# Optimization experiments

Measured on AMD Instinct MI355X. Metric: run time of the kernel, lower is better.

Reference implementation:

```python
import jax, jax.numpy as jnp
import numpy as np

B, T, C = 2, 2048, 1024
H, HS = 16, 64          # num_heads, head_size; H*HS == C
FF = 4 * C
EPS = 1e-5


def setup_inputs() -> dict:
    key = jax.random.key(0)
    ks = jax.random.split(key, 10)
    s = 0.02
    return {
        "x": jax.random.normal(ks[0], (B, T, C), dtype=jnp.float32),
        "Wq": jax.random.normal(ks[1], (H, C, HS), dtype=jnp.float32) * s,
        "Wk": jax.random.normal(ks[2], (H, C, HS), dtype=jnp.float32) * s,
        "Wv": jax.random.normal(ks[3], (H, C, HS), dtype=jnp.float32) * s,
        "p": jnp.ones((H,), dtype=jnp.float32),  # per-head learnable scale, init 1
        "Wproj": jax.random.normal(ks[4], (C, C), dtype=jnp.float32) * s,
        "W1": jax.random.normal(ks[5], (C, FF), dtype=jnp.float32) * s,
        "W2": jax.random.normal(ks[6], (FF, C), dtype=jnp.float32) * s,
        "ln1_w": jnp.ones((C,), dtype=jnp.float32),
        "ln1_b": jnp.zeros((C,), dtype=jnp.float32),
        "ln2_w": jnp.ones((C,), dtype=jnp.float32),
        "ln2_b": jnp.zeros((C,), dtype=jnp.float32),
    }


def _layernorm(x, w, b):
    mu = jnp.mean(x, axis=-1, keepdims=True)
    var = jnp.mean(jnp.square(x - mu), axis=-1, keepdims=True)
    return (x - mu) * jax.lax.rsqrt(var + EPS) * w + b


def reference(x, Wq, Wk, Wv, p, Wproj, W1, W2, ln1_w, ln1_b, ln2_w, ln2_b):
    # --- multi-head causal self-attention (dropout p=0 -> identity) ---
    h = _layernorm(x, ln1_w, ln1_b)
    q = jnp.einsum("btc,hcs->bhts", h, Wq)  # [B,H,T,HS]
    k = jnp.einsum("btc,hcs->bhts", h, Wk)
    v = jnp.einsum("btc,hcs->bhts", h, Wv)
    scale = p ** (-0.5)  # per-head scale, p init to 1
    wei = jnp.einsum("bhts,bhks->bhtk", q, k) * scale[None, :, None, None]
    causal = jnp.tril(jnp.ones((T, T), dtype=bool))
    wei = jnp.where(causal[None, None], wei, -jnp.inf)
    wei = jax.nn.softmax(wei, axis=-1)
    att = jnp.einsum("bhtk,bhks->bhts", wei, v)          # [B,H,T,HS]
    att = att.transpose(0, 2, 1, 3).reshape(B, T, C)     # concat heads
    sa = att @ Wproj
    x = x + sa
    # --- feed-forward (activation_id=0 -> ReLU) ---
    h2 = _layernorm(x, ln2_w, ln2_b)
    ff = jax.nn.relu(h2 @ W1) @ W2
    return x + ff
```

## Files before the change

kernel.cpp:

```cpp
#include <hip/hip_runtime.h>


typedef _Float16 f16;
typedef _Float16 f16x8 __attribute__((ext_vector_type(8)));
typedef _Float16 f16x4v __attribute__((ext_vector_type(4)));
typedef float f32x4 __attribute__((ext_vector_type(4)));

static constexpr int Tn = 2048;
static constexpr int Cn = 1024;
static constexpr int HSn = 64;

__device__ __forceinline__ void glds16(const f16* g, f16* l) {
    __builtin_amdgcn_global_load_lds((const __attribute__((address_space(1))) void*)g,
                                     (__attribute__((address_space(3))) void*)l,
                                     16, 0, 0);
}

__device__ __forceinline__ int xcd_swz(int wg, int nwg) {
    int cpx = nwg >> 3;
    return (wg & 7) * cpx + (wg >> 3);
}

__global__ __launch_bounds__(256) void ln_kernel(const float* __restrict__ x,
                                                 const float* __restrict__ w,
                                                 const float* __restrict__ b,
                                                 f16* __restrict__ out) {
    int row = blockIdx.x;
    const float* xr = x + (size_t)row * Cn;
    int tid = threadIdx.x, l = tid & 63, wv = tid >> 6;
    float4 v = *(const float4*)(xr + tid * 4);
    float s = v.x + v.y + v.z + v.w;
    float sq = v.x * v.x + v.y * v.y + v.z * v.z + v.w * v.w;
#pragma unroll
    for (int off = 32; off > 0; off >>= 1) {
        s += __shfl_down(s, off);
        sq += __shfl_down(sq, off);
    }
    __shared__ float red[8];
    if (l == 0) { red[wv] = s; red[wv + 4] = sq; }
    __syncthreads();
    float ts = red[0] + red[1] + red[2] + red[3];
    float tq = red[4] + red[5] + red[6] + red[7];
    float mean = ts * (1.0f / Cn);
    float var = tq * (1.0f / Cn) - mean * mean;
    float rstd = rsqrtf(var + 1e-5f);
    float4 wv4 = *(const float4*)(w + tid * 4);
    float4 bv4 = *(const float4*)(b + tid * 4);
    f16x4v o;
    o[0] = (f16)((v.x - mean) * rstd * wv4.x + bv4.x);
    o[1] = (f16)((v.y - mean) * rstd * wv4.y + bv4.y);
    o[2] = (f16)((v.z - mean) * rstd * wv4.z + bv4.z);
    o[3] = (f16)((v.w - mean) * rstd * wv4.w + bv4.w);
    *(f16x4v*)(out + (size_t)row * Cn + tid * 4) = o;
}

__global__ __launch_bounds__(256) void tr_cast_f32(const float* __restrict__ in, int irs,
                                                   f16* __restrict__ out, int ors) {
    __shared__ float tile[32][33];
    int r0 = blockIdx.x * 32, c0 = blockIdx.y * 32;
    int t = threadIdx.x;
    int rr = t >> 3, c4 = (t & 7) * 4;
    float4 v = *(const float4*)(in + (size_t)(r0 + rr) * irs + c0 + c4);
    tile[rr][c4] = v.x; tile[rr][c4 + 1] = v.y; tile[rr][c4 + 2] = v.z; tile[rr][c4 + 3] = v.w;
    __syncthreads();
    int cc = t >> 3, r4 = (t & 7) * 4;
    f16x4v o;
    o[0] = (f16)tile[r4][cc];
    o[1] = (f16)tile[r4 + 1][cc];
    o[2] = (f16)tile[r4 + 2][cc];
    o[3] = (f16)tile[r4 + 3][cc];
    *(f16x4v*)(out + (size_t)(c0 + cc) * ors + r0 + r4) = o;
}

__global__ __launch_bounds__(256) void tr_cast_qkv(const float* __restrict__ Wq,
                                                   const float* __restrict__ Wk,
                                                   const float* __restrict__ Wv,
                                                   f16* __restrict__ out) {
    int z = blockIdx.z;
    int qkv = z >> 4, h = z & 15;
    const float* in = (qkv == 0 ? Wq : qkv == 1 ? Wk : Wv) + (size_t)h * Cn * HSn;
    f16* o = out + (size_t)(qkv * Cn + h * HSn) * Cn;
    __shared__ float tile[32][33];
    int r0 = blockIdx.x * 32, c0 = blockIdx.y * 32;
    int t = threadIdx.x;
    int rr = t >> 3, c4 = (t & 7) * 4;
    float4 v = *(const float4*)(in + (size_t)(r0 + rr) * HSn + c0 + c4);
    tile[rr][c4] = v.x; tile[rr][c4 + 1] = v.y; tile[rr][c4 + 2] = v.z; tile[rr][c4 + 3] = v.w;
    __syncthreads();
    int cc = t >> 3, r4 = (t & 7) * 4;
    f16x4v ov;
    ov[0] = (f16)tile[r4][cc];
    ov[1] = (f16)tile[r4 + 1][cc];
    ov[2] = (f16)tile[r4 + 2][cc];
    ov[3] = (f16)tile[r4 + 3][cc];
    *(f16x4v*)(o + (size_t)(c0 + cc) * Cn + r0 + r4) = ov;
}

__global__ __launch_bounds__(256) void tr_vT(const f16* __restrict__ QKV, f16* __restrict__ vT) {
    int bh = blockIdx.z;
    int b = bh >> 4, h = bh & 15;
    const f16* in = QKV + (size_t)b * Tn * 3072 + 2048 + h * HSn;
    f16* out = vT + (size_t)bh * HSn * Tn;
    int r0 = blockIdx.x * 64;
    __shared__ __align__(16) f16 tile[64][72];
    int t = threadIdx.x;
#pragma unroll
    for (int i = 0; i < 2; i++) {
        int f = i * 256 + t;
        int rr = f >> 3, c8 = (f & 7) * 8;
        *(uint4*)(&tile[rr][c8]) = *(const uint4*)(in + (size_t)(r0 + rr) * 3072 + c8);
    }
    __syncthreads();
#pragma unroll
    for (int i = 0; i < 2; i++) {
        int f = i * 256 + t;
        int cc = f >> 3, r8 = (f & 7) * 8;
        union { f16 h[8]; uint4 v; } u;
#pragma unroll
        for (int j = 0; j < 8; j++) u.h[j] = tile[r8 + j][cc];
        *(uint4*)(out + (size_t)cc * Tn + r0 + r8) = u.v;
    }
}

template <int EPI>
__global__ __launch_bounds__(256) void gemm_bt(const f16* __restrict__ A, const f16* __restrict__ Bt,
                                               void* __restrict__ Cout, const float* __restrict__ resid,
                                               int M, int N, int K) {
    __shared__ __align__(16) f16 As[2][4096];
    __shared__ __align__(16) f16 Bs[2][4096];
    int nwgx = gridDim.x;
    int sw = xcd_swz(blockIdx.y * nwgx + blockIdx.x, nwgx * gridDim.y);
    int bm = sw % nwgx, bn = sw / nwgx;
    int tid = threadIdx.x, l = tid & 63, w = tid >> 6;
    int wr = w >> 1, wc = w & 1;
    f32x4 acc[4][4];
#pragma unroll
    for (int m = 0; m < 4; m++)
#pragma unroll
        for (int n = 0; n < 4; n++) acc[m][n] = f32x4{0.f, 0.f, 0.f, 0.f};

    const f16* ag = A + (size_t)(bm * 128 + (tid >> 2)) * K + (tid & 3) * 8;
    const f16* bg = Bt + (size_t)(bn * 128 + (tid >> 2)) * K + (tid & 3) * 8;
    const size_t half = (size_t)64 * K;
    int KT = K >> 5;
    int rbase = (wr * 64 + (l & 15)) * 32 + (l >> 4) * 8;
    int cbase = (wc * 64 + (l & 15)) * 32 + (l >> 4) * 8;

    auto stage = [&](int kt, int bf) {
        int k0 = kt * 32;
        glds16(ag + k0, &As[bf][w * 512]);
        glds16(ag + half + k0, &As[bf][2048 + w * 512]);
        glds16(bg + k0, &Bs[bf][w * 512]);
        glds16(bg + half + k0, &Bs[bf][2048 + w * 512]);
    };

    stage(0, 0);
    __syncthreads();
    for (int kt = 0; kt < KT; ++kt) {
        int cb = kt & 1;
        if (kt + 1 < KT) stage(kt + 1, cb ^ 1);
        f16x8 af[4], bfr[4];
#pragma unroll
        for (int m = 0; m < 4; m++) af[m] = *(const f16x8*)(&As[cb][rbase + m * 512]);
#pragma unroll
        for (int n = 0; n < 4; n++) bfr[n] = *(const f16x8*)(&Bs[cb][cbase + n * 512]);
#pragma unroll
        for (int m = 0; m < 4; m++)
#pragma unroll
            for (int n = 0; n < 4; n++)
                acc[m][n] = __builtin_amdgcn_mfma_f32_16x16x32_f16(af[m], bfr[n], acc[m][n], 0, 0, 0);
        __syncthreads();
    }

    int row0 = bm * 128 + wr * 64 + (l >> 4) * 4;
    int col0 = bn * 128 + wc * 64 + (l & 15);
#pragma unroll
    for (int m = 0; m < 4; m++) {
#pragma unroll
        for (int n = 0; n < 4; n++) {
#pragma unroll
            for (int r = 0; r < 4; r++) {
                size_t idx = (size_t)(row0 + m * 16 + r) * N + (col0 + n * 16);
                float v = acc[m][n][r];
                if constexpr (EPI == 0) ((f16*)Cout)[idx] = (f16)v;
                else if constexpr (EPI == 1) ((f16*)Cout)[idx] = (f16)fmaxf(v, 0.f);
                else ((float*)Cout)[idx] = v + resid[idx];
            }
        }
    }
}

template <int EPI>
__global__ __launch_bounds__(512) void gemm_ks(const f16* __restrict__ A, const f16* __restrict__ Bt,
                                               void* __restrict__ Cout, const float* __restrict__ resid,
                                               int M, int N, int K) {
    __shared__ __align__(16) char smem[65536];
    f16* As = (f16*)smem;
    f16* Bs = (f16*)(smem + 32768);
    int nwgx = gridDim.x;
    int sw = xcd_swz(blockIdx.y * nwgx + blockIdx.x, nwgx * gridDim.y);
    int bm = sw % nwgx, bn = sw / nwgx;
    int tid = threadIdx.x, l = tid & 63, w = tid >> 6;
    int grp = w >> 2, wl = w & 3;
    int wr = wl >> 1, wc = wl & 1;
    int Kh = K >> 1;
    int KT = Kh >> 5;

    f32x4 acc[4][4];
#pragma unroll
    for (int m = 0; m < 4; m++)
#pragma unroll
        for (int n = 0; n < 4; n++) acc[m][n] = f32x4{0.f, 0.f, 0.f, 0.f};

    const f16* agp = A + (size_t)(bm * 128 + wl * 16 + (l >> 2)) * K + grp * Kh + (l & 3) * 8;
    const f16* bgp = Bt + (size_t)(bn * 128 + wl * 16 + (l >> 2)) * K + grp * Kh + (l & 3) * 8;
    const size_t half = (size_t)64 * K;
    f16* Ab = As + grp * 8192;
    f16* Bb = Bs + grp * 8192;

    auto stage = [&](int kt, int bf) {
        size_t k0 = (size_t)kt * 32;
        glds16(agp + k0, Ab + bf * 4096 + wl * 512);
        glds16(agp + half + k0, Ab + bf * 4096 + 2048 + wl * 512);
        glds16(bgp + k0, Bb + bf * 4096 + wl * 512);
        glds16(bgp + half + k0, Bb + bf * 4096 + 2048 + wl * 512);
    };

    int rbase = (wr * 64 + (l & 15)) * 32 + (l >> 4) * 8;
    int cbase = (wc * 64 + (l & 15)) * 32 + (l >> 4) * 8;

    stage(0, 0);
    __syncthreads();
    for (int kt = 0; kt < KT; ++kt) {
        int cb = kt & 1;
        if (kt + 1 < KT) stage(kt + 1, cb ^ 1);
        f16x8 af[4], bfr[4];
#pragma unroll
        for (int m = 0; m < 4; m++) af[m] = *(const f16x8*)(Ab + cb * 4096 + rbase + m * 512);
#pragma unroll
        for (int n = 0; n < 4; n++) bfr[n] = *(const f16x8*)(Bb + cb * 4096 + cbase + n * 512);
#pragma unroll
        for (int m = 0; m < 4; m++)
#pragma unroll
            for (int n = 0; n < 4; n++)
                acc[m][n] = __builtin_amdgcn_mfma_f32_16x16x32_f16(af[m], bfr[n], acc[m][n], 0, 0, 0);
        __syncthreads();
    }

    float* red = (float*)smem;
#pragma unroll
    for (int m = 0; m < 4; m++) {
        if (grp == 1) {
#pragma unroll
            for (int n = 0; n < 4; n++)
                *(f32x4*)(red + wl * 1280 + l * 20 + n * 4) = acc[m][n];
        }
        __syncthreads();
        if (grp == 0) {
#pragma unroll
            for (int n = 0; n < 4; n++)
                acc[m][n] += *(const f32x4*)(red + wl * 1280 + l * 20 + n * 4);
        }
        __syncthreads();
    }

    if (grp == 0) {
        int row0 = bm * 128 + wr * 64 + (l >> 4) * 4;
        int col0 = bn * 128 + wc * 64 + (l & 15);
#pragma unroll
        for (int m = 0; m < 4; m++) {
#pragma unroll
            for (int n = 0; n < 4; n++) {
#pragma unroll
                for (int r = 0; r < 4; r++) {
                    size_t idx = (size_t)(row0 + m * 16 + r) * N + (col0 + n * 16);
                    float v = acc[m][n][r];
                    if constexpr (EPI == 0) ((f16*)Cout)[idx] = (f16)v;
                    else if constexpr (EPI == 1) ((f16*)Cout)[idx] = (f16)fmaxf(v, 0.f);
                    else ((float*)Cout)[idx] = v + resid[idx];
                }
            }
        }
    }
}

__global__ __launch_bounds__(256) void attn_kernel(const f16* __restrict__ QKV,
                                                   const f16* __restrict__ vT,
                                                   const float* __restrict__ p,
                                                   f16* __restrict__ att) {
    int sw = xcd_swz(blockIdx.x, gridDim.x);
    int pq = sw & 15, bh = sw >> 4;
    int b = bh >> 4, h = bh & 15;
    int tid = threadIdx.x, w = tid >> 6, l = tid & 63;
    float scale = rsqrtf(p[h]);

    __shared__ __align__(16) f16 Ks[2][4096];
    __shared__ __align__(16) f16 Vs[2][4096];
    __shared__ __align__(16) f16 Ps[4][16 * 80];
    f16* Pw = &Ps[w][0];

    int srow0 = tid >> 3;
    int c0 = (tid & 7) ^ (srow0 & 7);
    int srow1 = 32 + srow0;
    int c1 = (tid & 7) ^ (srow1 & 7);
    const f16* Kg = QKV + (size_t)b * Tn * 3072 + 1024 + h * HSn;
    const f16* Vg = vT + (size_t)bh * HSn * Tn;

    auto stageKV = [&](int kv0, int bf) {
        glds16(Kg + (size_t)(kv0 + srow0) * 3072 + c0 * 8, &Ks[bf][w * 512]);
        glds16(Kg + (size_t)(kv0 + srow1) * 3072 + c1 * 8, &Ks[bf][2048 + w * 512]);
        glds16(Vg + (size_t)srow0 * Tn + kv0 + c0 * 8, &Vs[bf][w * 512]);
        glds16(Vg + (size_t)srow1 * Tn + kv0 + c1 * 8, &Vs[bf][2048 + w * 512]);
    };

    for (int pass = 0; pass < 2; ++pass) {
        int qt = pass ? (31 - pq) : pq;
        int qg = qt * 64 + w * 16 + (l & 15);
        int qo = qt * 64 + w * 16 + (l >> 4) * 4;
        const f16* qptr = QKV + (size_t)(b * Tn + qg) * 3072 + h * HSn + (l >> 4) * 8;
        f16x8 qf0 = *(const f16x8*)(qptr);
        f16x8 qf1 = *(const f16x8*)(qptr + 32);

        f32x4 o[4];
#pragma unroll
        for (int nf = 0; nf < 4; nf++) o[nf] = f32x4{0.f, 0.f, 0.f, 0.f};
        float m_r = -1e30f, l_r = 0.f;

        int nt = qt + 1;
        stageKV(0, 0);
        __syncthreads();
        for (int t = 0; t < nt; ++t) {
            int cb = t & 1, kv0 = t * 64;
            if (t + 1 < nt) stageKV(kv0 + 64, cb ^ 1);
            const char* Kb = (const char*)&Ks[cb][0];
            const char* Vb = (const char*)&Vs[cb][0];
            f32x4 s[4];
#pragma unroll
            for (int n = 0; n < 4; n++) s[n] = f32x4{0.f, 0.f, 0.f, 0.f};
            __builtin_amdgcn_s_setprio(1);
#pragma unroll
            for (int n = 0; n < 4; n++) {
#pragma unroll
                for (int ks = 0; ks < 2; ks++) {
                    int boff = (n * 16 + (l & 15)) * 128 + (((ks * 32 + (l >> 4) * 8) * 2) ^ ((l & 7) << 4));
                    f16x8 kf = *(const f16x8*)(Kb + boff);
                    s[n] = __builtin_amdgcn_mfma_f32_16x16x32_f16(kf, ks == 0 ? qf0 : qf1, s[n], 0, 0, 0);
                }
            }
            __builtin_amdgcn_s_setprio(0);
            int rel = qg - kv0;
            float tmax = -1e30f;
#pragma unroll
            for (int n = 0; n < 4; n++) {
#pragma unroll
                for (int r = 0; r < 4; r++) {
                    int kvr = n * 16 + (l >> 4) * 4 + r;
                    float v = s[n][r] * scale;
                    v = (kvr <= rel) ? v : -1e30f;
                    s[n][r] = v;
                    tmax = fmaxf(tmax, v);
                }
            }
            tmax = fmaxf(tmax, __shfl_xor(tmax, 16));
            tmax = fmaxf(tmax, __shfl_xor(tmax, 32));
            float mnew = fmaxf(m_r, tmax);
            float alpha = __expf(m_r - mnew);
            m_r = mnew;
            float rsum = 0.f;
#pragma unroll
            for (int n = 0; n < 4; n++) {
                f16x4v pk;
#pragma unroll
                for (int r = 0; r < 4; r++) {
                    float e = __expf(s[n][r] - mnew);
                    rsum += e;
                    pk[r] = (f16)e;
                }
                *(f16x4v*)(&Pw[(l & 15) * 80 + n * 16 + (l >> 4) * 4]) = pk;
            }
            rsum += __shfl_xor(rsum, 16);
            rsum += __shfl_xor(rsum, 32);
            l_r = l_r * alpha + rsum;
            float ar[4];
#pragma unroll
            for (int r = 0; r < 4; r++) ar[r] = __shfl(alpha, (l >> 4) * 4 + r);
#pragma unroll
            for (int nf = 0; nf < 4; nf++)
#pragma unroll
                for (int r = 0; r < 4; r++) o[nf][r] *= ar[r];
            f16x8 pa0 = *(const f16x8*)(&Pw[(l & 15) * 80 + (l >> 4) * 8]);
            f16x8 pa1 = *(const f16x8*)(&Pw[(l & 15) * 80 + 32 + (l >> 4) * 8]);
            __builtin_amdgcn_s_setprio(1);
#pragma unroll
            for (int nf = 0; nf < 4; nf++) {
#pragma unroll
                for (int ks = 0; ks < 2; ks++) {
                    int boff = (nf * 16 + (l & 15)) * 128 + (((ks * 32 + (l >> 4) * 8) * 2) ^ ((l & 7) << 4));
                    f16x8 vf = *(const f16x8*)(Vb + boff);
                    o[nf] = __builtin_amdgcn_mfma_f32_16x16x32_f16(ks == 0 ? pa0 : pa1, vf, o[nf], 0, 0, 0);
                }
            }
            __builtin_amdgcn_s_setprio(0);
            __syncthreads();
        }
        float lro[4];
#pragma unroll
        for (int r = 0; r < 4; r++) lro[r] = __shfl(l_r, (l >> 4) * 4 + r);
#pragma unroll
        for (int nf = 0; nf < 4; nf++) {
#pragma unroll
            for (int r = 0; r < 4; r++) {
                float v = o[nf][r] / lro[r];
                att[(size_t)(b * Tn + qo + r) * Cn + h * HSn + nf * 16 + (l & 15)] = (f16)v;
            }
        }
    }
}

extern "C" void kernel_launch(void* const* d_in, const int* in_sizes, int n_in,
                              void* d_out, int out_size, void* d_ws, size_t ws_size,
                              hipStream_t stream) {
    const float* x = (const float*)d_in[0];
    const float* Wq = (const float*)d_in[1];
    const float* Wk = (const float*)d_in[2];
    const float* Wv = (const float*)d_in[3];
    const float* p = (const float*)d_in[4];
    const float* Wproj = (const float*)d_in[5];
    const float* W1 = (const float*)d_in[6];
    const float* W2 = (const float*)d_in[7];
    const float* ln1w = (const float*)d_in[8];
    const float* ln1b = (const float*)d_in[9];
    const float* ln2w = (const float*)d_in[10];
    const float* ln2b = (const float*)d_in[11];

    char* ws = (char*)d_ws;
    const size_t MB = 1ull << 20;
    f16* Wqkv_t = (f16*)(ws + 0 * MB);
    f16* Wproj_t = (f16*)(ws + 6 * MB);
    f16* W1_t = (f16*)(ws + 8 * MB);
    f16* W2_t = (f16*)(ws + 16 * MB);
    float* x1 = (float*)(ws + 24 * MB);
    f16* QKV = (f16*)(ws + 40 * MB);
    f16* h1 = (f16*)(ws + 64 * MB);
    f16* vTb = (f16*)(ws + 64 * MB);
    f16* attb = (f16*)(ws + 72 * MB);
    f16* h2 = attb;
    f16* ffh = QKV;
    float* out = (float*)d_out;

    tr_cast_qkv<<<dim3(32, 2, 48), 256, 0, stream>>>(Wq, Wk, Wv, Wqkv_t);
    tr_cast_f32<<<dim3(32, 32), 256, 0, stream>>>(Wproj, 1024, Wproj_t, 1024);
    tr_cast_f32<<<dim3(32, 128), 256, 0, stream>>>(W1, 4096, W1_t, 1024);
    tr_cast_f32<<<dim3(128, 32), 256, 0, stream>>>(W2, 1024, W2_t, 4096);

    ln_kernel<<<4096, 256, 0, stream>>>(x, ln1w, ln1b, h1);
    gemm_bt<0><<<dim3(32, 24), 256, 0, stream>>>(h1, Wqkv_t, QKV, nullptr, 4096, 3072, 1024);
    tr_vT<<<dim3(32, 1, 32), 256, 0, stream>>>(QKV, vTb);
    attn_kernel<<<512, 256, 0, stream>>>(QKV, vTb, p, attb);
    gemm_ks<2><<<dim3(32, 8), 512, 0, stream>>>(attb, Wproj_t, x1, x, 4096, 1024, 1024);
    ln_kernel<<<4096, 256, 0, stream>>>(x1, ln2w, ln2b, h2);
    gemm_bt<1><<<dim3(32, 32), 256, 0, stream>>>(h2, W1_t, ffh, nullptr, 4096, 4096, 1024);
    gemm_ks<2><<<dim3(32, 8), 512, 0, stream>>>(ffh, W2_t, out, x1, 4096, 1024, 4096);
}
```

Baseline: 262.0 us.

## Triple-buffer LDS staging with vmcnt waits and single barrier per iteration

Converts the double-buffered global->LDS pipelines in gemm_bt, gemm_ks and the attention kernel to a three-stage ring. Loads are issued two tiles ahead, and each iteration waits with an explicit s_waitcnt vmcnt plus one raw barrier instead of two __syncthreads. The aim is to hide more global-load latency behind MFMA work and to cut a barrier per iteration. The cost is 1.5x the LDS footprint, up to 96KB in gemm_ks, which may lower occupancy. Correctness also depends on the hand-counted vmcnt values and on whether the compiler honours the raw barrier ordering.

```diff
diff --git a/kernel.cpp b/kernel.cpp
--- a/kernel.cpp
+++ b/kernel.cpp
@@ -20,6 +20,8 @@
     int cpx = nwg >> 3;
     return (wg & 7) * cpx + (wg >> 3);
 }
+
+#define VMCNT(N) asm volatile("s_waitcnt vmcnt(" #N ")" ::: "memory")
 
 __global__ __launch_bounds__(256) void ln_kernel(const float* __restrict__ x,
                                                  const float* __restrict__ w,
@@ -126,8 +128,8 @@
 __global__ __launch_bounds__(256) void gemm_bt(const f16* __restrict__ A, const f16* __restrict__ Bt,
                                                void* __restrict__ Cout, const float* __restrict__ resid,
                                                int M, int N, int K) {
-    __shared__ __align__(16) f16 As[2][4096];
-    __shared__ __align__(16) f16 Bs[2][4096];
+    __shared__ __align__(16) f16 As[3][4096];
+    __shared__ __align__(16) f16 Bs[3][4096];
     int nwgx = gridDim.x;
     int sw = xcd_swz(blockIdx.y * nwgx + blockIdx.x, nwgx * gridDim.y);
     int bm = sw % nwgx, bn = sw / nwgx;
@@ -155,10 +157,13 @@
     };
 
     stage(0, 0);
-    __syncthreads();
+    if (KT > 1) stage(1, 1);
+    int cb = 0, nb = 2;
     for (int kt = 0; kt < KT; ++kt) {
-        int cb = kt & 1;
-        if (kt + 1 < KT) stage(kt + 1, cb ^ 1);
+        if (kt + 1 < KT) VMCNT(4);
+        else VMCNT(0);
+        __builtin_amdgcn_s_barrier();
+        if (kt + 2 < KT) { stage(kt + 2, nb); nb = (nb == 2) ? 0 : nb + 1; }
         f16x8 af[4], bfr[4];
 #pragma unroll
         for (int m = 0; m < 4; m++) af[m] = *(const f16x8*)(&As[cb][rbase + m * 512]);
@@ -169,7 +174,7 @@
 #pragma unroll
             for (int n = 0; n < 4; n++)
                 acc[m][n] = __builtin_amdgcn_mfma_f32_16x16x32_f16(af[m], bfr[n], acc[m][n], 0, 0, 0);
-        __syncthreads();
+        cb = (cb == 2) ? 0 : cb + 1;
     }
 
     int row0 = bm * 128 + wr * 64 + (l >> 4) * 4;
@@ -194,9 +199,9 @@
 __global__ __launch_bounds__(512) void gemm_ks(const f16* __restrict__ A, const f16* __restrict__ Bt,
                                                void* __restrict__ Cout, const float* __restrict__ resid,
                                                int M, int N, int K) {
-    __shared__ __align__(16) char smem[65536];
+    __shared__ __align__(16) char smem[98304];
     f16* As = (f16*)smem;
-    f16* Bs = (f16*)(smem + 32768);
+    f16* Bs = (f16*)(smem + 49152);
     int nwgx = gridDim.x;
     int sw = xcd_swz(blockIdx.y * nwgx + blockIdx.x, nwgx * gridDim.y);
     int bm = sw % nwgx, bn = sw / nwgx;
@@ -215,8 +220,8 @@
     const f16* agp = A + (size_t)(bm * 128 + wl * 16 + (l >> 2)) * K + grp * Kh + (l & 3) * 8;
     const f16* bgp = Bt + (size_t)(bn * 128 + wl * 16 + (l >> 2)) * K + grp * Kh + (l & 3) * 8;
     const size_t half = (size_t)64 * K;
-    f16* Ab = As + grp * 8192;
-    f16* Bb = Bs + grp * 8192;
+    f16* Ab = As + grp * 12288;
+    f16* Bb = Bs + grp * 12288;
 
     auto stage = [&](int kt, int bf) {
         size_t k0 = (size_t)kt * 32;
@@ -230,10 +235,13 @@
     int cbase = (wc * 64 + (l & 15)) * 32 + (l >> 4) * 8;
 
     stage(0, 0);
-    __syncthreads();
+    if (KT > 1) stage(1, 1);
+    int cb = 0, nb = 2;
     for (int kt = 0; kt < KT; ++kt) {
-        int cb = kt & 1;
-        if (kt + 1 < KT) stage(kt + 1, cb ^ 1);
+        if (kt + 1 < KT) VMCNT(4);
+        else VMCNT(0);
+        __builtin_amdgcn_s_barrier();
+        if (kt + 2 < KT) { stage(kt + 2, nb); nb = (nb == 2) ? 0 : nb + 1; }
         f16x8 af[4], bfr[4];
 #pragma unroll
         for (int m = 0; m < 4; m++) af[m] = *(const f16x8*)(Ab + cb * 4096 + rbase + m * 512);
@@ -244,8 +252,9 @@
 #pragma unroll
             for (int n = 0; n < 4; n++)
                 acc[m][n] = __builtin_amdgcn_mfma_f32_16x16x32_f16(af[m], bfr[n], acc[m][n], 0, 0, 0);
-        __syncthreads();
-    }
+        cb = (cb == 2) ? 0 : cb + 1;
+    }
+    __syncthreads();
 
     float* red = (float*)smem;
 #pragma unroll
@@ -294,8 +303,8 @@
     int tid = threadIdx.x, w = tid >> 6, l = tid & 63;
     float scale = rsqrtf(p[h]);
 
-    __shared__ __align__(16) f16 Ks[2][4096];
-    __shared__ __align__(16) f16 Vs[2][4096];
+    __shared__ __align__(16) f16 Ks[3][4096];
+    __shared__ __align__(16) f16 Vs[3][4096];
     __shared__ __align__(16) f16 Ps[4][16 * 80];
     f16* Pw = &Ps[w][0];
 
@@ -328,10 +337,14 @@
 
         int nt = qt + 1;
         stageKV(0, 0);
-        __syncthreads();
+        if (nt > 1) stageKV(64, 1);
+        int cb = 0, nb = 2;
         for (int t = 0; t < nt; ++t) {
-            int cb = t & 1, kv0 = t * 64;
-            if (t + 1 < nt) stageKV(kv0 + 64, cb ^ 1);
+            if (t + 1 < nt) VMCNT(4);
+            else VMCNT(0);
+            __builtin_amdgcn_s_barrier();
+            if (t + 2 < nt) { stageKV((t + 2) * 64, nb); nb = (nb == 2) ? 0 : nb + 1; }
+            int kv0 = t * 64;
             const char* Kb = (const char*)&Ks[cb][0];
             const char* Vb = (const char*)&Vs[cb][0];
             f32x4 s[4];
@@ -401,8 +414,9 @@
                 }
             }
             __builtin_amdgcn_s_setprio(0);
-            __syncthreads();
-        }
+            cb = (cb == 2) ? 0 : cb + 1;
+        }
+        __syncthreads();
         float lro[4];
 #pragma unroll
         for (int r = 0; r < 4; r++) lro[r] = __shfl(l_r, (l >> 4) * 4 + r);
```

Result: no change. 261.1 us (-0.4%).

## Fold softmax scale into Q, use exp2, lazy rescale, mask diagonal only, remap tiles

Applied to the files above, without the earlier changes.

The attention kernel pre-multiplies Q by scale*log2(e) in fp16 and switches to exp2f. The causal mask now applies only on the diagonal tile, and the running max and output are rescaled only when some row's max rises by more than 8. Both the GEMMs and attention replace the XCD swizzle with a fixed L2-oriented tile mapping. The risks are that the hardcoded grid width of 32 in the GEMM mapping may not match every launch, the fp16 scaling of Q loses some precision, and the lazy rescale allows exponentials up to 2^8 before the fp16 cast.

```diff
diff --git a/kernel.cpp b/kernel.cpp
--- a/kernel.cpp
+++ b/kernel.cpp
@@ -14,11 +14,6 @@
     __builtin_amdgcn_global_load_lds((const __attribute__((address_space(1))) void*)g,
                                      (__attribute__((address_space(3))) void*)l,
                                      16, 0, 0);
-}
-
-__device__ __forceinline__ int xcd_swz(int wg, int nwg) {
-    int cpx = nwg >> 3;
-    return (wg & 7) * cpx + (wg >> 3);
 }
 
 __global__ __launch_bounds__(256) void ln_kernel(const float* __restrict__ x,
@@ -122,15 +117,21 @@
     }
 }
 
+__device__ __forceinline__ void l2_map(int& bm, int& bn) {
+    int wg = blockIdx.y * 32 + blockIdx.x;
+    int x = wg & 7, idx = wg >> 3;
+    bm = x * 4 + (idx & 3);
+    bn = idx >> 2;
+}
+
 template <int EPI>
 __global__ __launch_bounds__(256) void gemm_bt(const f16* __restrict__ A, const f16* __restrict__ Bt,
                                                void* __restrict__ Cout, const float* __restrict__ resid,
                                                int M, int N, int K) {
     __shared__ __align__(16) f16 As[2][4096];
     __shared__ __align__(16) f16 Bs[2][4096];
-    int nwgx = gridDim.x;
-    int sw = xcd_swz(blockIdx.y * nwgx + blockIdx.x, nwgx * gridDim.y);
-    int bm = sw % nwgx, bn = sw / nwgx;
+    int bm, bn;
+    l2_map(bm, bn);
     int tid = threadIdx.x, l = tid & 63, w = tid >> 6;
     int wr = w >> 1, wc = w & 1;
     f32x4 acc[4][4];
@@ -197,9 +198,8 @@
     __shared__ __align__(16) char smem[65536];
     f16* As = (f16*)smem;
     f16* Bs = (f16*)(smem + 32768);
-    int nwgx = gridDim.x;
-    int sw = xcd_swz(blockIdx.y * nwgx + blockIdx.x, nwgx * gridDim.y);
-    int bm = sw % nwgx, bn = sw / nwgx;
+    int bm, bn;
+    l2_map(bm, bn);
     int tid = threadIdx.x, l = tid & 63, w = tid >> 6;
     int grp = w >> 2, wl = w & 3;
     int wr = wl >> 1, wc = wl & 1;
@@ -288,11 +288,13 @@
                                                    const f16* __restrict__ vT,
                                                    const float* __restrict__ p,
                                                    f16* __restrict__ att) {
-    int sw = xcd_swz(blockIdx.x, gridDim.x);
-    int pq = sw & 15, bh = sw >> 4;
+    int wg = blockIdx.x;
+    int x = wg & 7, idx = wg >> 3;
+    int bh = x * 4 + (idx & 3);
+    int pq = idx >> 2;
     int b = bh >> 4, h = bh & 15;
     int tid = threadIdx.x, w = tid >> 6, l = tid & 63;
-    float scale = rsqrtf(p[h]);
+    float sc2 = rsqrtf(p[h]) * 1.44269504f;
 
     __shared__ __align__(16) f16 Ks[2][4096];
     __shared__ __align__(16) f16 Vs[2][4096];
@@ -320,6 +322,9 @@
         const f16* qptr = QKV + (size_t)(b * Tn + qg) * 3072 + h * HSn + (l >> 4) * 8;
         f16x8 qf0 = *(const f16x8*)(qptr);
         f16x8 qf1 = *(const f16x8*)(qptr + 32);
+        f16 sch = (f16)sc2;
+#pragma unroll
+        for (int j = 0; j < 8; j++) { qf0[j] *= sch; qf1[j] *= sch; }
 
         f32x4 o[4];
 #pragma unroll
@@ -348,31 +353,43 @@
                 }
             }
             __builtin_amdgcn_s_setprio(0);
-            int rel = qg - kv0;
+            if (t == qt) {
+                int rel = qg - kv0;
+#pragma unroll
+                for (int n = 0; n < 4; n++)
+#pragma unroll
+                    for (int r = 0; r < 4; r++) {
+                        int kvr = n * 16 + (l >> 4) * 4 + r;
+                        if (kvr > rel) s[n][r] = -1e30f;
+                    }
+            }
             float tmax = -1e30f;
 #pragma unroll
-            for (int n = 0; n < 4; n++) {
-#pragma unroll
-                for (int r = 0; r < 4; r++) {
-                    int kvr = n * 16 + (l >> 4) * 4 + r;
-                    float v = s[n][r] * scale;
-                    v = (kvr <= rel) ? v : -1e30f;
-                    s[n][r] = v;
-                    tmax = fmaxf(tmax, v);
-                }
-            }
+            for (int n = 0; n < 4; n++)
+#pragma unroll
+                for (int r = 0; r < 4; r++) tmax = fmaxf(tmax, s[n][r]);
             tmax = fmaxf(tmax, __shfl_xor(tmax, 16));
             tmax = fmaxf(tmax, __shfl_xor(tmax, 32));
-            float mnew = fmaxf(m_r, tmax);
-            float alpha = __expf(m_r - mnew);
-            m_r = mnew;
+            float lmul = 1.f;
+            if (__any(tmax > m_r + 8.f)) {
+                float mnew = fmaxf(m_r, tmax);
+                lmul = exp2f(m_r - mnew);
+                m_r = mnew;
+                float ar[4];
+#pragma unroll
+                for (int r = 0; r < 4; r++) ar[r] = __shfl(lmul, (l >> 4) * 4 + r);
+#pragma unroll
+                for (int nf = 0; nf < 4; nf++)
+#pragma unroll
+                    for (int r = 0; r < 4; r++) o[nf][r] *= ar[r];
+            }
             float rsum = 0.f;
 #pragma unroll
             for (int n = 0; n < 4; n++) {
                 f16x4v pk;
 #pragma unroll
                 for (int r = 0; r < 4; r++) {
-                    float e = __expf(s[n][r] - mnew);
+                    float e = exp2f(s[n][r] - m_r);
                     rsum += e;
                     pk[r] = (f16)e;
                 }
@@ -380,14 +397,7 @@
             }
             rsum += __shfl_xor(rsum, 16);
             rsum += __shfl_xor(rsum, 32);
-            l_r = l_r * alpha + rsum;
-            float ar[4];
-#pragma unroll
-            for (int r = 0; r < 4; r++) ar[r] = __shfl(alpha, (l >> 4) * 4 + r);
-#pragma unroll
-            for (int nf = 0; nf < 4; nf++)
-#pragma unroll
-                for (int r = 0; r < 4; r++) o[nf][r] *= ar[r];
+            l_r = l_r * lmul + rsum;
             f16x8 pa0 = *(const f16x8*)(&Pw[(l & 15) * 80 + (l >> 4) * 8]);
             f16x8 pa1 = *(const f16x8*)(&Pw[(l & 15) * 80 + 32 + (l >> 4) * 8]);
             __builtin_amdgcn_s_setprio(1);
```

New measurement: 253.3 us. 3.3% less time.
